# Performance work log

Hardware: AMD Instinct MI355X
Metric: run time of the kernel (lower is better)

## Reference

```python
import jax, jax.numpy as jnp
import numpy as np

B, T, N, H = 256, 64, 128, 128  # batch, seq_len, num_tasks, hidden_dim


def setup_inputs() -> dict:
    key = jax.random.key(0)
    k = jax.random.split(key, 8)
    task_seq = jax.random.randint(k[0], (B, T), 0, N)
    status_seq = jax.random.randint(k[1], (B, T), 0, 3)
    raw = (jax.random.uniform(k[2], (N, N)) < 0.05).astype(jnp.float32)
    adj = raw + jnp.eye(N, dtype=jnp.float32)
    rs = adj.sum(axis=1, keepdims=True)
    adj = adj / jnp.where(rs == 0, 1.0, rs)
    s = np.float32(1.0 / np.sqrt(H))
    emb = jax.random.normal(k[3], (N * 3, H), jnp.float32) * s      # interaction_emb
    W_ih = jax.random.normal(k[4], (3 * H, 2 * H), jnp.float32) * s  # GRUCell weight_ih (r,z,n)
    W_hh = jax.random.normal(k[5], (3 * H, H), jnp.float32) * s      # GRUCell weight_hh
    b_ih = jnp.zeros((3 * H,), jnp.float32)
    b_hh = jnp.zeros((3 * H,), jnp.float32)
    w_pred = jax.random.normal(k[6], (H,), jnp.float32) * s          # predict_layer weight [1,H] -> [H]
    b_pred = jnp.zeros((), jnp.float32)                              # predict_layer bias
    return dict(task_seq=task_seq, status_seq=status_seq, adj=adj, emb=emb,
                W_ih=W_ih, W_hh=W_hh, b_ih=b_ih, b_hh=b_hh,
                w_pred=w_pred, b_pred=b_pred)


def _gru_cell(x, h, W_ih, W_hh, b_ih, b_hh):
    # torch.nn.GRUCell: gates ordered (reset, update, new)
    gi = x @ W_ih.T + b_ih
    gh = h @ W_hh.T + b_hh
    i_r, i_z, i_n = jnp.split(gi, 3, axis=-1)
    h_r, h_z, h_n = jnp.split(gh, 3, axis=-1)
    r = jax.nn.sigmoid(i_r + h_r)
    z = jax.nn.sigmoid(i_z + h_z)
    n = jnp.tanh(i_n + r * h_n)
    return (1.0 - z) * n + z * h


def reference(task_seq, status_seq, adj, emb, W_ih, W_hh, b_ih, b_hh, w_pred, b_pred):
    Bsz, _ = task_seq.shape
    Nt = adj.shape[0]
    Hd = emb.shape[1]
    b_idx = jnp.arange(Bsz)
    h0 = jnp.zeros((Bsz, Nt, Hd), emb.dtype)

    def step(h, ts):
        task, status = ts                                # [B], [B]
        x = emb[task * 3 + status]                       # [B,H] interaction embedding
        # original: full (adj @ h)[b, task]; identical math computing only needed row
        agg = jnp.einsum('bn,bnh->bh', adj[task], h)     # [B,H]
        prev = h[b_idx, task]                            # [B,H]
        new = _gru_cell(jnp.concatenate([x, agg], axis=1), prev, W_ih, W_hh, b_ih, b_hh)
        h = h.at[b_idx, task].set(new)                   # scatter updated target state
        logits = h @ w_pred + b_pred                     # [B,N] predict over all tasks
        return h, logits

    h_final, logits = jax.lax.scan(step, h0, (task_seq.T, status_seq.T))
    return jnp.transpose(logits, (1, 0, 2)), h_final     # ([B,T,N], [B,N,H])
```

## Files before the change

### kernel.cpp

```cpp
#include <hip/hip_runtime.h>

#define B_ 256
#define T_ 64
#define N_ 128
#define H_ 128
#define G3 384
#define K2 256

#define WS_G    0
#define WS_PW   (WS_G + G3*G3)
#define WS_WLT  (WS_PW + K2*G3)
#define WS_NZC  (WS_WLT + H_*G3)
#define WS_NZP  (WS_NZC + 128)

__global__ void build_mats(const float* __restrict__ W_ih,
                           const float* __restrict__ W_hh,
                           float* __restrict__ ws) {
    float* PW  = ws + WS_PW;
    float* WLT = ws + WS_WLT;
    int idx = blockIdx.x * blockDim.x + threadIdx.x;
    const int total_pw = K2 * G3;
    if (idx < total_pw) {
        int k = idx / G3, j = idx % G3;
        PW[idx] = (k < H_) ? W_ih[j * K2 + H_ + k] : W_hh[j * H_ + (k - H_)];
    } else {
        int idx2 = idx - total_pw;
        if (idx2 < H_ * G3) {
            int k = idx2 / G3, j = idx2 % G3;
            WLT[idx2] = W_ih[j * K2 + k];
        }
    }
}

__global__ void build_G(const float* __restrict__ emb,
                        const float* __restrict__ b_ih,
                        float* __restrict__ ws) {
    __shared__ float es[H_];
    const float* WLT = ws + WS_WLT;
    float* G = ws + WS_G;
    const int e = blockIdx.x;
    const int j = threadIdx.x;
    if (j < H_) es[j] = emb[e * H_ + j];
    __syncthreads();
    float acc = b_ih[j];
    #pragma unroll 8
    for (int k = 0; k < H_; ++k) acc += WLT[k * G3 + j] * es[k];
    G[e * G3 + j] = acc;
}

__global__ void build_nz(const float* __restrict__ adj, float* __restrict__ ws) {
    __shared__ float row[N_];
    const int r = blockIdx.x;
    row[threadIdx.x] = adj[r * N_ + threadIdx.x];
    __syncthreads();
    if (threadIdx.x == 0) {
        int*  nzc = (int*)(ws + WS_NZC);
        int2* nzp = (int2*)(ws + WS_NZP);
        int cnt = 0;
        for (int n = 0; n < N_; ++n) {
            float w = row[n];
            if (w != 0.0f) { nzp[r * N_ + cnt] = make_int2(n, __float_as_int(w)); ++cnt; }
        }
        int cnt4 = (cnt + 3) & ~3;
        for (int i = cnt; i < cnt4; ++i) nzp[r * N_ + i] = make_int2(0, 0);
        nzc[r] = cnt;
    }
}

__global__ void __launch_bounds__(512) gkt_main(
        const int* __restrict__ task_seq, const int* __restrict__ status_seq,
        const float* __restrict__ b_hh,   const float* __restrict__ w_pred,
        const float* __restrict__ b_pred, const float* __restrict__ ws,
        float* __restrict__ out) {
    __shared__ __align__(16) float h_lds[N_ * H_];
    __shared__ float4 vbuf4[K2 / 4];
    __shared__ float  pl[4 * G3];
    __shared__ float  red[H_];
    __shared__ float  Ll[N_];
    __shared__ int2   nzl[2][N_];
    __shared__ int    nzc_l[2];

    const int b   = blockIdx.x;
    const int tid = threadIdx.x;
    const int t   = tid & 127;
    const int q   = tid >> 7;

    const float* G   = ws + WS_G;
    const float* PW  = ws + WS_PW;
    const int*   nzc = (const int*)(ws + WS_NZC);
    const int2*  nzp = (const int2*)(ws + WS_NZP);

    float wr[64], wz[64], wn[64];
    {
        const float* base = PW + (q * 64) * G3 + t;
        #pragma unroll
        for (int kk = 0; kk < 64; ++kk) {
            wr[kk] = base[kk * G3];
            wz[kk] = base[kk * G3 + 128];
            wn[kk] = base[kk * G3 + 256];
        }
    }
    const float bp = b_pred[0];
    float bhr = 0.f, bhz = 0.f, bhn = 0.f, wpt = 0.f;
    if (q == 0) { bhr = b_hh[t]; bhz = b_hh[128 + t]; bhn = b_hh[256 + t]; wpt = w_pred[t]; }

    for (int i = tid; i < N_ * H_; i += 512) h_lds[i] = 0.0f;
    if (tid < N_) Ll[tid] = bp;
    if (q == 1) {
        int t0 = task_seq[b * T_];
        nzl[0][t] = nzp[t0 * N_ + t];
        if (t == 0) nzc_l[0] = nzc[t0];
    }
    __syncthreads();

    float* vb = (float*)vbuf4;

    for (int s = 0; s < T_; ++s) {
        const int cur = s & 1, nxt = cur ^ 1;
        const int task = task_seq[b * T_ + s];
        const int stat = status_seq[b * T_ + s];
        float g0 = 0.f, g1 = 0.f, g2 = 0.f;

        if (q == 0) {
            const int e = task * 3 + stat;
            g0 = G[e * G3 + t];
            g1 = G[e * G3 + 128 + t];
            g2 = G[e * G3 + 256 + t];
            float acc = 0.0f;
            const int cnt4 = (nzc_l[cur] + 3) & ~3;
            for (int i = 0; i < cnt4; i += 4) {
                int2 p0 = nzl[cur][i + 0], p1 = nzl[cur][i + 1];
                int2 p2 = nzl[cur][i + 2], p3 = nzl[cur][i + 3];
                acc += __int_as_float(p0.y) * h_lds[p0.x * H_ + t];
                acc += __int_as_float(p1.y) * h_lds[p1.x * H_ + t];
                acc += __int_as_float(p2.y) * h_lds[p2.x * H_ + t];
                acc += __int_as_float(p3.y) * h_lds[p3.x * H_ + t];
            }
            vb[t] = acc;
        } else if (q == 1) {
            vb[128 + t] = h_lds[task * H_ + t];
        } else if (q == 2) {
            if (s > 0) out[(size_t)b * T_ * N_ + (size_t)(s - 1) * N_ + t] = Ll[t];
        }
        __syncthreads();

        {
            float pr = 0.f, pz = 0.f, pn = 0.f;
            const float* vq = vb + q * 64;
            #pragma unroll
            for (int kk = 0; kk < 64; kk += 4) {
                const float4 v = *(const float4*)(vq + kk);
                pr += wr[kk] * v.x + wr[kk + 1] * v.y + wr[kk + 2] * v.z + wr[kk + 3] * v.w;
                pz += wz[kk] * v.x + wz[kk + 1] * v.y + wz[kk + 2] * v.z + wz[kk + 3] * v.w;
                pn += wn[kk] * v.x + wn[kk + 1] * v.y + wn[kk + 2] * v.z + wn[kk + 3] * v.w;
            }
            pl[q * G3 + t]       = pr;
            pl[q * G3 + 128 + t] = pz;
            pl[q * G3 + 256 + t] = pn;
        }
        __syncthreads();

        if (q == 0) {
            float sr = g0 + bhr + pl[0*G3 + t] + pl[1*G3 + t] + pl[2*G3 + t] + pl[3*G3 + t];
            float sz = g1 + bhz + pl[0*G3 + 128 + t] + pl[1*G3 + 128 + t]
                                + pl[2*G3 + 128 + t] + pl[3*G3 + 128 + t];
            float in_ = g2 + pl[0*G3 + 256 + t] + pl[1*G3 + 256 + t];
            float hn_ = bhn + pl[2*G3 + 256 + t] + pl[3*G3 + 256 + t];
            float r = 1.0f / (1.0f + expf(-sr));
            float z = 1.0f / (1.0f + expf(-sz));
            float n = tanhf(in_ + r * hn_);
            float prev = h_lds[task * H_ + t];
            float hnew = (1.0f - z) * n + z * prev;
            h_lds[task * H_ + t] = hnew;
            red[t] = hnew * wpt;
        } else if (q == 1) {
            if (s + 1 < T_) {
                int tn = task_seq[b * T_ + s + 1];
                nzl[nxt][t] = nzp[tn * N_ + t];
                if (t == 0) nzc_l[nxt] = nzc[tn];
            }
        }
        __syncthreads();

        if (tid < 64) {
            float x = red[tid] + red[tid + 64];
            #pragma unroll
            for (int off = 32; off > 0; off >>= 1) x += __shfl_xor(x, off, 64);
            if (tid == 0) Ll[task] = x + bp;
        }
        __syncthreads();
    }

    if (q == 2) out[(size_t)b * T_ * N_ + (size_t)(T_ - 1) * N_ + t] = Ll[t];
    {
        float4* dst = (float4*)(out + (size_t)B_ * T_ * N_ + (size_t)b * N_ * H_);
        const float4* src = (const float4*)h_lds;
        for (int i = tid; i < N_ * H_ / 4; i += 512) dst[i] = src[i];
    }
}

extern "C" void kernel_launch(void* const* d_in, const int* in_sizes, int n_in,
                              void* d_out, int out_size, void* d_ws, size_t ws_size,
                              hipStream_t stream) {
    const int*   task = (const int*)d_in[0];
    const int*   stat = (const int*)d_in[1];
    const float* adj  = (const float*)d_in[2];
    const float* emb  = (const float*)d_in[3];
    const float* Wih  = (const float*)d_in[4];
    const float* Whh  = (const float*)d_in[5];
    const float* bih  = (const float*)d_in[6];
    const float* bhh  = (const float*)d_in[7];
    const float* wp   = (const float*)d_in[8];
    const float* bp   = (const float*)d_in[9];
    float* out = (float*)d_out;
    float* ws  = (float*)d_ws;

    build_mats<<<576, 256, 0, stream>>>(Wih, Whh, ws);
    build_G  <<<384, 384, 0, stream>>>(emb, bih, ws);
    build_nz <<<128, 128, 0, stream>>>(adj, ws);
    gkt_main <<<256, 512, 0, stream>>>(task, stat, bhh, wp, bp, ws, out);
}
```

Baseline: 215.9 us.

## Halve per-step barriers by computing next-step aggregation in GRU phase; merge prep kernels

Restructures the recurrent loop so each timestep uses two barriers instead of four. The second half-block recomputes the GRU output redundantly and uses it to build the next step's neighbour aggregation, substituting the freshly updated row. The logit reduction is deferred into the next step's first phase. Task and status sequences are staged in LDS, and the three preprocessing kernels are fused into one launch that reads W_ih directly instead of going through a transposed copy. The kernel also gains __launch_bounds__(512,2); with 192 weight registers per thread, this may constrain registers and cause spills.

```diff
diff --git a/kernel.cpp b/kernel.cpp
--- a/kernel.cpp
+++ b/kernel.cpp
@@ -9,76 +9,67 @@
 
 #define WS_G    0
 #define WS_PW   (WS_G + G3*G3)
-#define WS_WLT  (WS_PW + K2*G3)
-#define WS_NZC  (WS_WLT + H_*G3)
+#define WS_NZC  (WS_PW + K2*G3)
 #define WS_NZP  (WS_NZC + 128)
 
-__global__ void build_mats(const float* __restrict__ W_ih,
-                           const float* __restrict__ W_hh,
-                           float* __restrict__ ws) {
-    float* PW  = ws + WS_PW;
-    float* WLT = ws + WS_WLT;
-    int idx = blockIdx.x * blockDim.x + threadIdx.x;
-    const int total_pw = K2 * G3;
-    if (idx < total_pw) {
-        int k = idx / G3, j = idx % G3;
-        PW[idx] = (k < H_) ? W_ih[j * K2 + H_ + k] : W_hh[j * H_ + (k - H_)];
+__global__ void __launch_bounds__(384) prep(
+        const float* __restrict__ W_ih, const float* __restrict__ W_hh,
+        const float* __restrict__ emb,  const float* __restrict__ b_ih,
+        const float* __restrict__ adj,  float* __restrict__ ws) {
+    const int bid = blockIdx.x;
+    if (bid < 384) {
+        __shared__ float es[H_];
+        const int e = bid, j = threadIdx.x;
+        if (j < H_) es[j] = emb[e * H_ + j];
+        __syncthreads();
+        float acc = b_ih[j];
+        const float4* wrow = (const float4*)(W_ih + j * K2);
+        #pragma unroll 8
+        for (int i = 0; i < 32; ++i) {
+            float4 w = wrow[i];
+            acc += w.x * es[4*i];
+            acc += w.y * es[4*i + 1];
+            acc += w.z * es[4*i + 2];
+            acc += w.w * es[4*i + 3];
+        }
+        (ws + WS_G)[e * G3 + j] = acc;
+    } else if (bid < 512) {
+        __shared__ float row[N_];
+        const int r = bid - 384;
+        if (threadIdx.x < N_) row[threadIdx.x] = adj[r * N_ + threadIdx.x];
+        __syncthreads();
+        if (threadIdx.x == 0) {
+            int*  nzc = (int*)(ws + WS_NZC);
+            int2* nzp = (int2*)(ws + WS_NZP);
+            int cnt = 0;
+            for (int n = 0; n < N_; ++n) {
+                float w = row[n];
+                if (w != 0.0f) { nzp[r * N_ + cnt] = make_int2(n, __float_as_int(w)); ++cnt; }
+            }
+            int cnt4 = (cnt + 3) & ~3;
+            for (int i = cnt; i < cnt4; ++i) nzp[r * N_ + i] = make_int2(0, 0);
+            nzc[r] = cnt;
+        }
     } else {
-        int idx2 = idx - total_pw;
-        if (idx2 < H_ * G3) {
-            int k = idx2 / G3, j = idx2 % G3;
-            WLT[idx2] = W_ih[j * K2 + k];
-        }
+        const int k = bid - 512, j = threadIdx.x;
+        (ws + WS_PW)[k * G3 + j] = (k < H_) ? W_ih[j * K2 + H_ + k]
+                                            : W_hh[j * H_ + (k - H_)];
     }
 }
 
-__global__ void build_G(const float* __restrict__ emb,
-                        const float* __restrict__ b_ih,
-                        float* __restrict__ ws) {
-    __shared__ float es[H_];
-    const float* WLT = ws + WS_WLT;
-    float* G = ws + WS_G;
-    const int e = blockIdx.x;
-    const int j = threadIdx.x;
-    if (j < H_) es[j] = emb[e * H_ + j];
-    __syncthreads();
-    float acc = b_ih[j];
-    #pragma unroll 8
-    for (int k = 0; k < H_; ++k) acc += WLT[k * G3 + j] * es[k];
-    G[e * G3 + j] = acc;
-}
-
-__global__ void build_nz(const float* __restrict__ adj, float* __restrict__ ws) {
-    __shared__ float row[N_];
-    const int r = blockIdx.x;
-    row[threadIdx.x] = adj[r * N_ + threadIdx.x];
-    __syncthreads();
-    if (threadIdx.x == 0) {
-        int*  nzc = (int*)(ws + WS_NZC);
-        int2* nzp = (int2*)(ws + WS_NZP);
-        int cnt = 0;
-        for (int n = 0; n < N_; ++n) {
-            float w = row[n];
-            if (w != 0.0f) { nzp[r * N_ + cnt] = make_int2(n, __float_as_int(w)); ++cnt; }
-        }
-        int cnt4 = (cnt + 3) & ~3;
-        for (int i = cnt; i < cnt4; ++i) nzp[r * N_ + i] = make_int2(0, 0);
-        nzc[r] = cnt;
-    }
-}
-
-__global__ void __launch_bounds__(512) gkt_main(
+__global__ void __launch_bounds__(512, 2) gkt_main(
         const int* __restrict__ task_seq, const int* __restrict__ status_seq,
         const float* __restrict__ b_hh,   const float* __restrict__ w_pred,
         const float* __restrict__ b_pred, const float* __restrict__ ws,
         float* __restrict__ out) {
     __shared__ __align__(16) float h_lds[N_ * H_];
-    __shared__ float4 vbuf4[K2 / 4];
-    __shared__ float  pl[4 * G3];
-    __shared__ float  red[H_];
-    __shared__ float  Ll[N_];
-    __shared__ int2   nzl[2][N_];
-    __shared__ int    nzc_l[2];
+    __shared__ __align__(16) float aggbuf[H_];
+    __shared__ float pl[4 * G3];
+    __shared__ float red[H_];
+    __shared__ float Ll[N_];
+    __shared__ int2  nzbuf[N_];
+    __shared__ int   nz_cnt;
+    __shared__ int   tasks_l[T_], stats_l[T_];
 
     const int b   = blockIdx.x;
     const int tid = threadIdx.x;
@@ -102,54 +93,27 @@
     }
     const float bp = b_pred[0];
     float bhr = 0.f, bhz = 0.f, bhn = 0.f, wpt = 0.f;
-    if (q == 0) { bhr = b_hh[t]; bhz = b_hh[128 + t]; bhn = b_hh[256 + t]; wpt = w_pred[t]; }
+    if (q < 2) { bhr = b_hh[t]; bhz = b_hh[128 + t]; bhn = b_hh[256 + t]; }
+    if (q == 0) wpt = w_pred[t];
 
     for (int i = tid; i < N_ * H_; i += 512) h_lds[i] = 0.0f;
-    if (tid < N_) Ll[tid] = bp;
-    if (q == 1) {
-        int t0 = task_seq[b * T_];
-        nzl[0][t] = nzp[t0 * N_ + t];
-        if (t == 0) nzc_l[0] = nzc[t0];
-    }
+    if (tid < T_)            tasks_l[tid]       = task_seq[b * T_ + tid];
+    else if (tid < 2 * T_)   stats_l[tid - T_]  = status_seq[b * T_ + (tid - T_)];
+    if (tid < N_) { Ll[tid] = bp; aggbuf[tid] = 0.0f; }
     __syncthreads();
 
-    float* vb = (float*)vbuf4;
-
     for (int s = 0; s < T_; ++s) {
-        const int cur = s & 1, nxt = cur ^ 1;
-        const int task = task_seq[b * T_ + s];
-        const int stat = status_seq[b * T_ + s];
-        float g0 = 0.f, g1 = 0.f, g2 = 0.f;
-
-        if (q == 0) {
-            const int e = task * 3 + stat;
-            g0 = G[e * G3 + t];
-            g1 = G[e * G3 + 128 + t];
-            g2 = G[e * G3 + 256 + t];
-            float acc = 0.0f;
-            const int cnt4 = (nzc_l[cur] + 3) & ~3;
-            for (int i = 0; i < cnt4; i += 4) {
-                int2 p0 = nzl[cur][i + 0], p1 = nzl[cur][i + 1];
-                int2 p2 = nzl[cur][i + 2], p3 = nzl[cur][i + 3];
-                acc += __int_as_float(p0.y) * h_lds[p0.x * H_ + t];
-                acc += __int_as_float(p1.y) * h_lds[p1.x * H_ + t];
-                acc += __int_as_float(p2.y) * h_lds[p2.x * H_ + t];
-                acc += __int_as_float(p3.y) * h_lds[p3.x * H_ + t];
-            }
-            vb[t] = acc;
-        } else if (q == 1) {
-            vb[128 + t] = h_lds[task * H_ + t];
-        } else if (q == 2) {
-            if (s > 0) out[(size_t)b * T_ * N_ + (size_t)(s - 1) * N_ + t] = Ll[t];
-        }
-        __syncthreads();
-
+        const int task = tasks_l[s];
+
+        float prevreg = 0.f;
+        if (q < 2) prevreg = h_lds[task * H_ + t];
         {
+            const float* vbase = (q < 2) ? (aggbuf + q * 64)
+                                         : (h_lds + task * H_ + (q - 2) * 64);
             float pr = 0.f, pz = 0.f, pn = 0.f;
-            const float* vq = vb + q * 64;
             #pragma unroll
             for (int kk = 0; kk < 64; kk += 4) {
-                const float4 v = *(const float4*)(vq + kk);
+                const float4 v = *(const float4*)(vbase + kk);
                 pr += wr[kk] * v.x + wr[kk + 1] * v.y + wr[kk + 2] * v.z + wr[kk + 3] * v.w;
                 pz += wz[kk] * v.x + wz[kk + 1] * v.y + wz[kk + 2] * v.z + wz[kk + 3] * v.w;
                 pn += wn[kk] * v.x + wn[kk + 1] * v.y + wn[kk + 2] * v.z + wn[kk + 3] * v.w;
@@ -158,40 +122,66 @@
             pl[q * G3 + 128 + t] = pz;
             pl[q * G3 + 256 + t] = pn;
         }
-        __syncthreads();
-
-        if (q == 0) {
-            float sr = g0 + bhr + pl[0*G3 + t] + pl[1*G3 + t] + pl[2*G3 + t] + pl[3*G3 + t];
-            float sz = g1 + bhz + pl[0*G3 + 128 + t] + pl[1*G3 + 128 + t]
-                                + pl[2*G3 + 128 + t] + pl[3*G3 + 128 + t];
+        if (q == 3 && s + 1 < T_) {
+            const int tn = tasks_l[s + 1];
+            nzbuf[t] = nzp[tn * N_ + t];
+            if (t == 0) nz_cnt = nzc[tn];
+        }
+        if (tid < 64 && s > 0) {
+            float x = red[tid] + red[tid + 64];
+            #pragma unroll
+            for (int off = 32; off > 0; off >>= 1) x += __shfl_xor(x, off, 64);
+            if (tid == 0) Ll[tasks_l[s - 1]] = x + bp;
+        }
+        __syncthreads();
+
+        if (q < 2) {
+            const int e = task * 3 + stats_l[s];
+            const float g0 = G[e * G3 + t];
+            const float g1 = G[e * G3 + 128 + t];
+            const float g2 = G[e * G3 + 256 + t];
+            float sr  = g0 + bhr + pl[0*G3 + t] + pl[1*G3 + t] + pl[2*G3 + t] + pl[3*G3 + t];
+            float sz  = g1 + bhz + pl[0*G3 + 128 + t] + pl[1*G3 + 128 + t]
+                                 + pl[2*G3 + 128 + t] + pl[3*G3 + 128 + t];
             float in_ = g2 + pl[0*G3 + 256 + t] + pl[1*G3 + 256 + t];
             float hn_ = bhn + pl[2*G3 + 256 + t] + pl[3*G3 + 256 + t];
             float r = 1.0f / (1.0f + expf(-sr));
             float z = 1.0f / (1.0f + expf(-sz));
             float n = tanhf(in_ + r * hn_);
-            float prev = h_lds[task * H_ + t];
-            float hnew = (1.0f - z) * n + z * prev;
-            h_lds[task * H_ + t] = hnew;
-            red[t] = hnew * wpt;
-        } else if (q == 1) {
-            if (s + 1 < T_) {
-                int tn = task_seq[b * T_ + s + 1];
-                nzl[nxt][t] = nzp[tn * N_ + t];
-                if (t == 0) nzc_l[nxt] = nzc[tn];
+            float hnew = (1.0f - z) * n + z * prevreg;
+            if (q == 0) {
+                h_lds[task * H_ + t] = hnew;
+                red[t] = hnew * wpt;
+            } else if (s + 1 < T_) {
+                float acc = 0.0f;
+                const int cnt4 = (nz_cnt + 3) & ~3;
+                for (int i = 0; i < cnt4; i += 4) {
+                    int2 p0 = nzbuf[i], p1 = nzbuf[i+1], p2 = nzbuf[i+2], p3 = nzbuf[i+3];
+                    float h0 = (p0.x == task) ? hnew : h_lds[p0.x * H_ + t];
+                    float h1 = (p1.x == task) ? hnew : h_lds[p1.x * H_ + t];
+                    float h2 = (p2.x == task) ? hnew : h_lds[p2.x * H_ + t];
+                    float h3 = (p3.x == task) ? hnew : h_lds[p3.x * H_ + t];
+                    acc += __int_as_float(p0.y) * h0;
+                    acc += __int_as_float(p1.y) * h1;
+                    acc += __int_as_float(p2.y) * h2;
+                    acc += __int_as_float(p3.y) * h3;
+                }
+                aggbuf[t] = acc;
             }
-        }
-        __syncthreads();
-
-        if (tid < 64) {
-            float x = red[tid] + red[tid + 64];
-            #pragma unroll
-            for (int off = 32; off > 0; off >>= 1) x += __shfl_xor(x, off, 64);
-            if (tid == 0) Ll[task] = x + bp;
-        }
-        __syncthreads();
-    }
-
-    if (q == 2) out[(size_t)b * T_ * N_ + (size_t)(T_ - 1) * N_ + t] = Ll[t];
+        } else if (q == 2) {
+            if (s > 0) out[(size_t)b * T_ * N_ + (size_t)(s - 1) * N_ + t] = Ll[t];
+        }
+        __syncthreads();
+    }
+
+    if (tid < 64) {
+        float x = red[tid] + red[tid + 64];
+        #pragma unroll
+        for (int off = 32; off > 0; off >>= 1) x += __shfl_xor(x, off, 64);
+        if (tid == 0) Ll[tasks_l[T_ - 1]] = x + bp;
+    }
+    __syncthreads();
+    if (tid < N_) out[(size_t)b * T_ * N_ + (size_t)(T_ - 1) * N_ + tid] = Ll[tid];
     {
         float4* dst = (float4*)(out + (size_t)B_ * T_ * N_ + (size_t)b * N_ * H_);
         const float4* src = (const float4*)h_lds;
@@ -208,15 +198,13 @@
     const float* emb  = (const float*)d_in[3];
     const float* Wih  = (const float*)d_in[4];
     const float* Whh  = (const float*)d_in[5];
-    const float* bih  = (const float*)d_in[6];
     const float* bhh  = (const float*)d_in[7];
     const float* wp   = (const float*)d_in[8];
     const float* bp   = (const float*)d_in[9];
+    const float* bih  = (const float*)d_in[6];
     float* out = (float*)d_out;
     float* ws  = (float*)d_ws;
 
-    build_mats<<<576, 256, 0, stream>>>(Wih, Whh, ws);
-    build_G  <<<384, 384, 0, stream>>>(emb, bih, ws);
-    build_nz <<<128, 128, 0, stream>>>(adj, ws);
-    gkt_main <<<256, 512, 0, stream>>>(task, stat, bhh, wp, bp, ws, out);
+    prep    <<<768, 384, 0, stream>>>(Wih, Whh, emb, bih, adj, ws);
+    gkt_main<<<256, 512, 0, stream>>>(task, stat, bhh, wp, bp, ws, out);
 }
```

Result: no change. 217.5 us (+0.7%).
